# Optimization experiments

Hardware: AMD Instinct MI355X
Metric: run time of the kernel (lower is better)

## Reference

```python
import jax, jax.numpy as jnp
import numpy as np

DIM = 512
HEADS = 8
HEAD_DIM = DIM // HEADS
SCALE = HEAD_DIM ** -0.5
B, H, W = 8, 64, 64


def rotate_every_two(x):
    # interleaved pair rotation: (x0,x1,x2,x3,...) -> (-x1,x0,-x3,x2,...)
    x1 = x[..., ::2]
    x2 = x[..., 1::2]
    return jnp.stack([-x2, x1], axis=-1).reshape(x.shape)


def theta_shift(x, sin, cos):
    return x * cos + rotate_every_two(x) * sin


def setup_inputs() -> dict:
    key = jax.random.key(0)
    ks = jax.random.split(key, 6)
    N = H * W
    x = jax.random.normal(ks[0], (B, DIM, H, W), jnp.float32)
    sin = jax.random.uniform(ks[1], (N, HEAD_DIM), jnp.float32, minval=-1.0, maxval=1.0)
    cos = jax.random.uniform(ks[2], (N, HEAD_DIM), jnp.float32, minval=-1.0, maxval=1.0)
    w_qkvo = jax.random.normal(ks[3], (4 * DIM, DIM), jnp.float32) * (DIM ** -0.5)
    b_qkvo = jnp.zeros((4 * DIM,), jnp.float32)
    w_lepe = jax.random.normal(ks[4], (DIM, 1, 5, 5), jnp.float32) * 0.1
    b_lepe = jnp.zeros((DIM,), jnp.float32)
    w_proj = jax.random.normal(ks[5], (DIM, DIM), jnp.float32) * (DIM ** -0.5)
    b_proj = jnp.zeros((DIM,), jnp.float32)
    return dict(x=x, sin=sin, cos=cos, w_qkvo=w_qkvo, b_qkvo=b_qkvo,
                w_lepe=w_lepe, b_lepe=b_lepe, w_proj=w_proj, b_proj=b_proj)


def reference(x, sin, cos, w_qkvo, b_qkvo, w_lepe, b_lepe, w_proj, b_proj):
    Bx, C, Hx, Wx = x.shape
    N = Hx * Wx
    # 1x1 conv qkvo projection
    qkvo = jnp.einsum('bchw,oc->bohw', x, w_qkvo) + b_qkvo[None, :, None, None]
    qkv = qkvo[:, :3 * DIM]
    o = qkvo[:, 3 * DIM:]
    # depthwise 5x5 lepe on v (spatial layout)
    v_sp = qkv[:, 2 * DIM:3 * DIM]
    lepe = jax.lax.conv_general_dilated(
        v_sp, w_lepe, window_strides=(1, 1), padding=((2, 2), (2, 2)),
        dimension_numbers=('NCHW', 'OIHW', 'NCHW'), feature_group_count=DIM,
    ) + b_lepe[None, :, None, None]
    # b (3 n d) h w -> (3, b, n, N, d)
    qkv5 = qkv.reshape(Bx, 3, HEADS, HEAD_DIM, N).transpose(1, 0, 2, 4, 3)
    q, k, v = qkv5[0], qkv5[1], qkv5[2]
    q = jax.nn.elu(q) + 1.0
    k = jax.nn.elu(k) + 1.0
    # softmax-gated eff weighting of k
    q_mean = q.mean(axis=-2, keepdims=True)                       # (b,n,1,d)
    eff = SCALE * jnp.einsum('bnod,bntd->bnot', q_mean, k)        # (b,n,1,N)
    eff = jax.nn.softmax(eff, axis=-1).swapaxes(-1, -2)           # (b,n,N,1)
    k = k * eff * N
    # RoPE-style rotation
    q_rope = theta_shift(q, sin, cos)
    k_rope = theta_shift(k, sin, cos)
    # normalizer z (uses un-rotated q, gated k)
    z = 1.0 / (jnp.einsum('bntd,bnod->bnto', q, k.mean(axis=-2, keepdims=True)) + 1e-6)  # (b,n,N,1)
    # linear-attention kv accumulation (d x d)
    inv_sqrt_n = N ** -0.5
    kv = jnp.einsum('bntd,bnte->bnde', k_rope * inv_sqrt_n, v * inv_sqrt_n)  # (b,n,d,d)
    res = jnp.einsum('bntd,bnde->bnte', q_rope, kv) * z            # (b,n,N,d)
    # b n N d -> b (n d) h w
    res = res.transpose(0, 1, 3, 2).reshape(Bx, DIM, Hx, Wx)
    res = res + lepe
    out = jnp.einsum('bchw,oc->bohw', res * o, w_proj) + b_proj[None, :, None, None]
    return out
```

## Files before the change

### kernel.cpp

```cpp
#include <hip/hip_runtime.h>
#include <math.h>

#define N_SP 4096
#define DIMC 512
#define HEADS 8
#define HD 64
#define CH_STRIDE 1536

typedef __attribute__((ext_vector_type(8))) short short8;
typedef __attribute__((ext_vector_type(4))) float f32x4;

__device__ __forceinline__ float elu1(float x) { return x > 0.f ? x + 1.f : expf(x); }

__device__ __forceinline__ float waveSum(float v) {
#pragma unroll
    for (int o = 1; o < 64; o <<= 1) v += __shfl_xor(v, o);
    return v;
}
__device__ __forceinline__ float waveMax(float v) {
#pragma unroll
    for (int o = 1; o < 64; o <<= 1) v = fmaxf(v, __shfl_xor(v, o));
    return v;
}

__device__ __forceinline__ unsigned short f2bf(float f) {
    union { float f; unsigned u; } v; v.f = f;
    unsigned r = v.u + 0x7fffu + ((v.u >> 16) & 1u);
    return (unsigned short)(r >> 16);
}
__device__ __forceinline__ unsigned pk2(float lo, float hi) {
    return (unsigned)f2bf(lo) | ((unsigned)f2bf(hi) << 16);
}

template<bool GATED>
__global__ __launch_bounds__(256) void gemm_bf16(
    const float* __restrict__ W, const float* __restrict__ bias,
    const float* __restrict__ Bsrc, const float* __restrict__ Gsrc,
    float* __restrict__ C, int src_cstride, int dst_cstride)
{
    __shared__ unsigned short Ws[4096];
    __shared__ unsigned short Xs[4096];
    int b  = blockIdx.z;
    int bo = blockIdx.y * 128;
    int bn = blockIdx.x * 128;
    const float* Bb = Bsrc + (size_t)b * src_cstride * N_SP + bn;
    const float* Gb = GATED ? (Gsrc + (size_t)b * src_cstride * N_SP + bn) : nullptr;
    int tid  = threadIdx.x;
    int lane = tid & 63;
    int wid  = tid >> 6;
    int wm = (wid >> 1) * 64, wn = (wid & 1) * 64;
    int quad = lane >> 4, l16 = lane & 15;
    int sm = tid >> 1, sp = tid & 1;
    int xn = tid & 127, xk0 = tid >> 7;

    f32x4 acc[4][4];
#pragma unroll
    for (int i = 0; i < 4; i++)
#pragma unroll
        for (int j = 0; j < 4; j++) acc[i][j] = f32x4{0.f, 0.f, 0.f, 0.f};

    for (int c0 = 0; c0 < DIMC; c0 += 32) {
        const float* wp = W + (size_t)(bo + sm) * DIMC + c0 + sp * 16;
        float4 w0 = *(const float4*)(wp);
        float4 w1 = *(const float4*)(wp + 4);
        float4 w2 = *(const float4*)(wp + 8);
        float4 w3 = *(const float4*)(wp + 12);
        float xv[2][8];
#pragma unroll
        for (int g = 0; g < 2; g++) {
            int kb = xk0 + g * 2;
            const float* xp = Bb + (size_t)(c0 + kb * 8) * N_SP + xn;
#pragma unroll
            for (int i = 0; i < 8; i++) xv[g][i] = xp[(size_t)i * N_SP];
            if (GATED) {
                const float* gp = Gb + (size_t)(c0 + kb * 8) * N_SP + xn;
#pragma unroll
                for (int i = 0; i < 8; i++) xv[g][i] *= gp[(size_t)i * N_SP];
            }
        }
        if (c0) __syncthreads();
        {
            uint4 a, bq;
            a.x  = pk2(w0.x, w0.y); a.y  = pk2(w0.z, w0.w);
            a.z  = pk2(w1.x, w1.y); a.w  = pk2(w1.z, w1.w);
            bq.x = pk2(w2.x, w2.y); bq.y = pk2(w2.z, w2.w);
            bq.z = pk2(w3.x, w3.y); bq.w = pk2(w3.z, w3.w);
            *(uint4*)&Ws[(2 * sp)     * 1024 + sm * 8] = a;
            *(uint4*)&Ws[(2 * sp + 1) * 1024 + sm * 8] = bq;
        }
#pragma unroll
        for (int g = 0; g < 2; g++) {
            int kb = xk0 + g * 2;
            uint4 a;
            a.x = pk2(xv[g][0], xv[g][1]); a.y = pk2(xv[g][2], xv[g][3]);
            a.z = pk2(xv[g][4], xv[g][5]); a.w = pk2(xv[g][6], xv[g][7]);
            *(uint4*)&Xs[kb * 1024 + xn * 8] = a;
        }
        __syncthreads();
        short8 af[4], bf[4];
#pragma unroll
        for (int i = 0; i < 4; i++) {
            af[i] = *(const short8*)&Ws[quad * 1024 + (wm + i * 16 + l16) * 8];
            bf[i] = *(const short8*)&Xs[quad * 1024 + (wn + i * 16 + l16) * 8];
        }
#pragma unroll
        for (int i = 0; i < 4; i++)
#pragma unroll
            for (int j = 0; j < 4; j++)
                acc[i][j] = __builtin_amdgcn_mfma_f32_16x16x32_bf16(
                    af[i], bf[j], acc[i][j], 0, 0, 0);
    }
    float* Cb = C + (size_t)b * dst_cstride * N_SP;
#pragma unroll
    for (int i = 0; i < 4; i++) {
        int row0 = bo + wm + i * 16 + quad * 4;
#pragma unroll
        for (int r = 0; r < 4; r++) {
            float bi = bias[row0 + r];
            float* cr = Cb + (size_t)(row0 + r) * N_SP + bn + wn + l16;
#pragma unroll
            for (int j = 0; j < 4; j++)
                cr[j * 16] = acc[i][j][r] + bi;
        }
    }
}

__global__ __launch_bounds__(256) void qmean_kernel(
    const float* __restrict__ QKV, float* __restrict__ qmean)
{
    int d = blockIdx.x, h = blockIdx.y, b = blockIdx.z;
    const float* row = QKV + ((size_t)b * CH_STRIDE + h * 64 + d) * N_SP;
    int tid = threadIdx.x;
    float s = 0.f;
#pragma unroll
    for (int j = 0; j < 4; j++) {
        float4 v = ((const float4*)row)[j * 256 + tid];
        s += elu1(v.x) + elu1(v.y) + elu1(v.z) + elu1(v.w);
    }
    s = waveSum(s);
    __shared__ float red[4];
    if ((tid & 63) == 0) red[tid >> 6] = s;
    __syncthreads();
    if (tid == 0)
        qmean[((size_t)b * 8 + h) * 64 + d] = (red[0] + red[1] + red[2] + red[3]) * (1.f / N_SP);
}

__global__ __launch_bounds__(256) void logits_kernel(
    const float* __restrict__ QKV, const float* __restrict__ qmean,
    float* __restrict__ eff)
{
    int tc = blockIdx.x, h = blockIdx.y, b = blockIdx.z;
    int tid = threadIdx.x;
    int t = tc * 256 + tid;
    __shared__ float qm[64];
    if (tid < 64) qm[tid] = qmean[((size_t)b * 8 + h) * 64 + tid];
    __syncthreads();
    const float* kb = QKV + ((size_t)b * CH_STRIDE + 512 + h * 64) * N_SP;
    float s = 0.f;
#pragma unroll 8
    for (int d = 0; d < 64; d++) s += qm[d] * elu1(kb[(size_t)d * N_SP + t]);
    eff[((size_t)b * 8 + h) * N_SP + t] = 0.125f * s;
}

__global__ __launch_bounds__(256) void softmax_kernel(float* __restrict__ eff)
{
    int bh = blockIdx.x;
    float* row = eff + (size_t)bh * N_SP;
    int tid = threadIdx.x;
    float4 v[4];
#pragma unroll
    for (int j = 0; j < 4; j++) v[j] = ((float4*)row)[j * 256 + tid];
    float m = -1e30f;
#pragma unroll
    for (int j = 0; j < 4; j++)
        m = fmaxf(m, fmaxf(fmaxf(v[j].x, v[j].y), fmaxf(v[j].z, v[j].w)));
    m = waveMax(m);
    __shared__ float red[8];
    if ((tid & 63) == 0) red[tid >> 6] = m;
    __syncthreads();
    m = fmaxf(fmaxf(red[0], red[1]), fmaxf(red[2], red[3]));
    float s = 0.f;
#pragma unroll
    for (int j = 0; j < 4; j++) {
        v[j].x = expf(v[j].x - m); v[j].y = expf(v[j].y - m);
        v[j].z = expf(v[j].z - m); v[j].w = expf(v[j].w - m);
        s += v[j].x + v[j].y + v[j].z + v[j].w;
    }
    float ws = waveSum(s);
    if ((tid & 63) == 0) red[4 + (tid >> 6)] = ws;
    __syncthreads();
    float tot = red[4] + red[5] + red[6] + red[7];
    float sc = (float)N_SP / tot;
#pragma unroll
    for (int j = 0; j < 4; j++) {
        v[j].x *= sc; v[j].y *= sc; v[j].z *= sc; v[j].w *= sc;
        ((float4*)row)[j * 256 + tid] = v[j];
    }
}

__global__ __launch_bounds__(256) void kv_kernel(
    const float* __restrict__ QKV, const float* __restrict__ eff,
    const float* __restrict__ sinp, const float* __restrict__ cosp,
    float* __restrict__ kv, float* __restrict__ kmean)
{
    int sp = blockIdx.x;
    int h = blockIdx.y, b = blockIdx.z;
    int bh = b * 8 + h;
    int tid = threadIdx.x;
    int r = tid >> 2, quad = tid & 3;
    const float* krow = QKV + ((size_t)b * CH_STRIDE + 512 + h * 64 + r) * N_SP;
    const float* vrow = QKV + ((size_t)b * CH_STRIDE + 1024 + h * 64 + r) * N_SP;
    const float* prow = eff + (size_t)bh * N_SP;
    __shared__ float ksr[64 * 65];
    __shared__ float vs[64 * 65];
    int dg = tid >> 4, eg = tid & 15;
    float acc[4][4];
#pragma unroll
    for (int i = 0; i < 4; i++)
#pragma unroll
        for (int j = 0; j < 4; j++) acc[i][j] = 0.f;
    float km = 0.f;
    float sgn = (r & 1) ? 1.f : -1.f;

    for (int c = 0; c < 8; c++) {
        int t0 = sp * 512 + c * 64;
        int tb = t0 + quad * 16;
        float kx[16], vv[16];
#pragma unroll
        for (int i4 = 0; i4 < 4; i4++) {
            float4 kf = *(const float4*)(krow + tb + i4 * 4);
            float4 pf = *(const float4*)(prow + tb + i4 * 4);
            float4 vf = *(const float4*)(vrow + tb + i4 * 4);
            kx[i4 * 4 + 0] = elu1(kf.x) * pf.x;
            kx[i4 * 4 + 1] = elu1(kf.y) * pf.y;
            kx[i4 * 4 + 2] = elu1(kf.z) * pf.z;
            kx[i4 * 4 + 3] = elu1(kf.w) * pf.w;
            vv[i4 * 4 + 0] = vf.x; vv[i4 * 4 + 1] = vf.y;
            vv[i4 * 4 + 2] = vf.z; vv[i4 * 4 + 3] = vf.w;
        }
#pragma unroll
        for (int i = 0; i < 16; i++) km += kx[i];
        __syncthreads();
#pragma unroll
        for (int i = 0; i < 16; i++) {
            float partner = __shfl_xor(kx[i], 4);
            int t = tb + i;
            float sv = sinp[(size_t)t * 64 + r];
            float cv = cosp[(size_t)t * 64 + r];
            float kr = kx[i] * cv + sgn * partner * sv;
            ksr[r * 65 + (t - t0)] = kr;
            vs[r * 65 + (t - t0)] = vv[i];
        }
        __syncthreads();
#pragma unroll 8
        for (int t = 0; t < 64; t++) {
            float a[4], bb[4];
#pragma unroll
            for (int i = 0; i < 4; i++) a[i] = ksr[(dg * 4 + i) * 65 + t];
#pragma unroll
            for (int j = 0; j < 4; j++) bb[j] = vs[(eg * 4 + j) * 65 + t];
#pragma unroll
            for (int i = 0; i < 4; i++)
#pragma unroll
                for (int j = 0; j < 4; j++) acc[i][j] += a[i] * bb[j];
        }
    }
#pragma unroll
    for (int i = 0; i < 4; i++)
#pragma unroll
        for (int j = 0; j < 4; j++)
            atomicAdd(&kv[((size_t)bh * 64 + dg * 4 + i) * 64 + eg * 4 + j],
                      acc[i][j] * (1.f / N_SP));
    km += __shfl_xor(km, 1);
    km += __shfl_xor(km, 2);
    if (quad == 0) atomicAdd(&kmean[(size_t)bh * 64 + r], km * (1.f / N_SP));
}

__global__ __launch_bounds__(256) void res_kernel(
    const float* __restrict__ QKV, const float* __restrict__ kv,
    const float* __restrict__ kmean,
    const float* __restrict__ sinp, const float* __restrict__ cosp,
    float* __restrict__ res)
{
    int tc = blockIdx.x;
    int h = blockIdx.y, b = blockIdx.z;
    int bh = b * 8 + h;
    int tid = threadIdx.x;
    int t0 = tc * 64;
    __shared__ float qsr[64 * 65];
    __shared__ float qse[64 * 65];
    __shared__ float kvs[64 * 65];
    __shared__ float zs[64];
    __shared__ float kms[64];
#pragma unroll
    for (int j = 0; j < 16; j++) {
        int lin = j * 256 + tid;
        kvs[(lin >> 6) * 65 + (lin & 63)] = kv[(size_t)bh * 4096 + lin];
    }
    if (tid < 64) kms[tid] = kmean[(size_t)bh * 64 + tid];

    int r = tid >> 2, quad = tid & 3;
    const float* qrow = QKV + ((size_t)b * CH_STRIDE + h * 64 + r) * N_SP;
    float sgn = (r & 1) ? 1.f : -1.f;
    int tb = t0 + quad * 16;
#pragma unroll
    for (int i4 = 0; i4 < 4; i4++) {
        float4 qf = *(const float4*)(qrow + tb + i4 * 4);
        float qe[4] = { elu1(qf.x), elu1(qf.y), elu1(qf.z), elu1(qf.w) };
#pragma unroll
        for (int ii = 0; ii < 4; ii++) {
            float partner = __shfl_xor(qe[ii], 4);
            int t = tb + i4 * 4 + ii;
            float sv = sinp[(size_t)t * 64 + r];
            float cv = cosp[(size_t)t * 64 + r];
            qse[r * 65 + (t - t0)] = qe[ii];
            qsr[r * 65 + (t - t0)] = qe[ii] * cv + sgn * partner * sv;
        }
    }
    __syncthreads();
    if (tid < 64) {
        float s = 0.f;
#pragma unroll 8
        for (int d = 0; d < 64; d++) s += qse[d * 65 + tid] * kms[d];
        zs[tid] = 1.f / (s + 1e-6f);
    }
    __syncthreads();

    int eg = tid >> 4, tg = tid & 15;
    float acc[4][4];
#pragma unroll
    for (int j = 0; j < 4; j++)
#pragma unroll
        for (int i = 0; i < 4; i++) acc[j][i] = 0.f;
#pragma unroll 4
    for (int d = 0; d < 64; d++) {
        float qv[4], kvv[4];
#pragma unroll
        for (int i = 0; i < 4; i++) qv[i] = qsr[d * 65 + tg * 4 + i];
#pragma unroll
        for (int j = 0; j < 4; j++) kvv[j] = kvs[d * 65 + eg * 4 + j];
#pragma unroll
        for (int j = 0; j < 4; j++)
#pragma unroll
            for (int i = 0; i < 4; i++) acc[j][i] += kvv[j] * qv[i];
    }
    float* rb = res + ((size_t)b * CH_STRIDE + 512 + h * 64) * N_SP;
#pragma unroll
    for (int j = 0; j < 4; j++) {
        float4 o4;
        o4.x = acc[j][0] * zs[tg * 4 + 0];
        o4.y = acc[j][1] * zs[tg * 4 + 1];
        o4.z = acc[j][2] * zs[tg * 4 + 2];
        o4.w = acc[j][3] * zs[tg * 4 + 3];
        *(float4*)(rb + (size_t)(eg * 4 + j) * N_SP + t0 + tg * 4) = o4;
    }
}

#define LPS 73
__global__ __launch_bounds__(256) void lepe_kernel(
    const float* __restrict__ QKV, const float* __restrict__ wl,
    const float* __restrict__ bl, float* __restrict__ res)
{
    int c = blockIdx.x & 511;
    int b = blockIdx.x >> 9;
    __shared__ float img[68 * LPS];
    int tid = threadIdx.x;
    const float* vb = QKV + ((size_t)b * CH_STRIDE + 1024 + c) * N_SP;

    for (int i = tid; i < 68 * LPS; i += 256) img[i] = 0.f;
    __syncthreads();
#pragma unroll
    for (int i = 0; i < 4; i++) {
        int p = i * 256 + tid;
        float4 v4 = ((const float4*)vb)[p];
        int y = p >> 4;
        int x = (p & 15) * 4;
        float* dst = &img[(y + 2) * LPS + (x + 2)];
        dst[0] = v4.x; dst[1] = v4.y; dst[2] = v4.z; dst[3] = v4.w;
    }
    float w[25];
    const float* wc = wl + c * 25;
#pragma unroll
    for (int i = 0; i < 25; i++) w[i] = wc[i];
    float bias = bl[c];
    __syncthreads();

    int y  = tid >> 2;
    int x0 = (tid & 3) * 16;
    float acc[16];
#pragma unroll
    for (int u = 0; u < 16; u++) acc[u] = bias;
#pragma unroll
    for (int i = 0; i < 5; i++) {
        float rowv[20];
#pragma unroll
        for (int q = 0; q < 20; q++)
            rowv[q] = img[(y + i) * LPS + x0 + q];
#pragma unroll
        for (int j = 0; j < 5; j++)
#pragma unroll
            for (int u = 0; u < 16; u++)
                acc[u] += rowv[u + j] * w[i * 5 + j];
    }
    float* rr = res + ((size_t)b * CH_STRIDE + 512 + c) * N_SP + y * 64 + x0;
#pragma unroll
    for (int q = 0; q < 4; q++) {
        float4 r4 = *(const float4*)&rr[q * 4];
        r4.x += acc[q * 4 + 0]; r4.y += acc[q * 4 + 1];
        r4.z += acc[q * 4 + 2]; r4.w += acc[q * 4 + 3];
        *(float4*)&rr[q * 4] = r4;
    }
}

extern "C" void kernel_launch(void* const* d_in, const int* in_sizes, int n_in,
                              void* d_out, int out_size, void* d_ws, size_t ws_size,
                              hipStream_t stream)
{
    const float* x      = (const float*)d_in[0];
    const float* sinp   = (const float*)d_in[1];
    const float* cosp   = (const float*)d_in[2];
    const float* w_qkvo = (const float*)d_in[3];
    const float* b_qkvo = (const float*)d_in[4];
    const float* w_lepe = (const float*)d_in[5];
    const float* b_lepe = (const float*)d_in[6];
    const float* w_proj = (const float*)d_in[7];
    const float* b_proj = (const float*)d_in[8];
    float* out = (float*)d_out;
    float* ws  = (float*)d_ws;

    float* qkv   = ws;
    float* eff   = ws + 50331648;
    float* qmean = ws + 50593792;
    float* kmean = ws + 50597888;
    float* kv    = ws + 50601984;

    hipMemsetAsync(kmean, 0, (4096 + 262144) * sizeof(float), stream);

    gemm_bf16<false><<<dim3(32, 12, 8), 256, 0, stream>>>(
        w_qkvo, b_qkvo, x, nullptr, qkv, DIMC, CH_STRIDE);
    qmean_kernel<<<dim3(64, 8, 8), 256, 0, stream>>>(qkv, qmean);
    logits_kernel<<<dim3(16, 8, 8), 256, 0, stream>>>(qkv, qmean, eff);
    softmax_kernel<<<64, 256, 0, stream>>>(eff);
    kv_kernel<<<dim3(8, 8, 8), 256, 0, stream>>>(qkv, eff, sinp, cosp, kv, kmean);
    res_kernel<<<dim3(64, 8, 8), 256, 0, stream>>>(qkv, kv, kmean, sinp, cosp, qkv);
    lepe_kernel<<<4096, 256, 0, stream>>>(qkv, w_lepe, b_lepe, qkv);
    gemm_bf16<false><<<dim3(32, 4, 8), 256, 0, stream>>>(
        w_qkvo + 1536 * DIMC, b_qkvo + 1536, x, nullptr, qkv, DIMC, CH_STRIDE);
    gemm_bf16<true><<<dim3(32, 4, 8), 256, 0, stream>>>(
        w_proj, b_proj, qkv + (size_t)512 * N_SP, qkv, out, CH_STRIDE, DIMC);
}
```

Measured before the change: 570.8 us.

## Pre-convert x and weights to bf16 and load GEMM tiles via global_load_lds

```diff
diff --git a/kernel.cpp b/kernel.cpp
--- a/kernel.cpp
+++ b/kernel.cpp
@@ -9,6 +9,7 @@
 
 typedef __attribute__((ext_vector_type(8))) short short8;
 typedef __attribute__((ext_vector_type(4))) float f32x4;
+typedef unsigned short ushortx;
 
 __device__ __forceinline__ float elu1(float x) { return x > 0.f ? x + 1.f : expf(x); }
 
@@ -32,8 +33,104 @@
     return (unsigned)f2bf(lo) | ((unsigned)f2bf(hi) << 16);
 }
 
-template<bool GATED>
-__global__ __launch_bounds__(256) void gemm_bf16(
+__device__ __forceinline__ void gl_lds16(const unsigned short* g, unsigned short* l) {
+    __builtin_amdgcn_global_load_lds(
+        (const __attribute__((address_space(1))) unsigned int*)g,
+        (__attribute__((address_space(3))) unsigned int*)l, 16, 0, 0);
+}
+
+__global__ __launch_bounds__(256) void cvt_xT(
+    const float* __restrict__ x, unsigned short* __restrict__ xT)
+{
+    int n  = blockIdx.x * 256 + threadIdx.x;
+    int c0 = blockIdx.y * 128;
+    int b  = blockIdx.z;
+    const float* xb = x + ((size_t)b * DIMC + c0) * N_SP + n;
+    unsigned short* xo = xT + ((size_t)b * N_SP + n) * DIMC + c0;
+    for (int cc = 0; cc < 128; cc += 8) {
+        float v[8];
+#pragma unroll
+        for (int i = 0; i < 8; i++) v[i] = xb[(size_t)(cc + i) * N_SP];
+        uint4 p;
+        p.x = pk2(v[0], v[1]); p.y = pk2(v[2], v[3]);
+        p.z = pk2(v[4], v[5]); p.w = pk2(v[6], v[7]);
+        *(uint4*)&xo[cc] = p;
+    }
+}
+
+__global__ __launch_bounds__(256) void cvt_wb(
+    const float* __restrict__ w, unsigned short* __restrict__ wb, int n4)
+{
+    int i = blockIdx.x * 256 + threadIdx.x;
+    if (i < n4) {
+        float4 v = ((const float4*)w)[i];
+        uint2 p; p.x = pk2(v.x, v.y); p.y = pk2(v.z, v.w);
+        *(uint2*)&wb[(size_t)i * 4] = p;
+    }
+}
+
+__global__ __launch_bounds__(256) void gemm_bb(
+    const unsigned short* __restrict__ Wb, const float* __restrict__ bias,
+    const unsigned short* __restrict__ xT, float* __restrict__ C,
+    int dst_cstride)
+{
+    __shared__ __align__(16) unsigned short Ws[4096];
+    __shared__ __align__(16) unsigned short Xs[4096];
+    int b  = blockIdx.z;
+    int bo = blockIdx.y * 128;
+    int bn = blockIdx.x * 128;
+    const unsigned short* Xb = xT + ((size_t)b * N_SP + bn) * DIMC;
+    int tid  = threadIdx.x;
+    int lane = tid & 63;
+    int wid  = tid >> 6;
+    int wm = (wid >> 1) * 64, wn = (wid & 1) * 64;
+    int quad = lane >> 4, l16 = lane & 15;
+
+    f32x4 acc[4][4];
+#pragma unroll
+    for (int i = 0; i < 4; i++)
+#pragma unroll
+        for (int j = 0; j < 4; j++) acc[i][j] = f32x4{0.f, 0.f, 0.f, 0.f};
+
+    for (int c0 = 0; c0 < DIMC; c0 += 32) {
+        if (c0) __syncthreads();
+#pragma unroll
+        for (int r = 0; r < 2; r++) {
+            gl_lds16(Wb + (size_t)(bo + r * 64 + lane) * DIMC + c0 + wid * 8,
+                     &Ws[wid * 1024 + r * 512]);
+            gl_lds16(Xb + (size_t)(r * 64 + lane) * DIMC + c0 + wid * 8,
+                     &Xs[wid * 1024 + r * 512]);
+        }
+        __syncthreads();
+        short8 af[4], bf[4];
+#pragma unroll
+        for (int i = 0; i < 4; i++) {
+            af[i] = *(const short8*)&Ws[quad * 1024 + (wm + i * 16 + l16) * 8];
+            bf[i] = *(const short8*)&Xs[quad * 1024 + (wn + i * 16 + l16) * 8];
+        }
+#pragma unroll
+        for (int i = 0; i < 4; i++)
+#pragma unroll
+            for (int j = 0; j < 4; j++)
+                acc[i][j] = __builtin_amdgcn_mfma_f32_16x16x32_bf16(
+                    af[i], bf[j], acc[i][j], 0, 0, 0);
+    }
+    float* Cb = C + (size_t)b * dst_cstride * N_SP;
+#pragma unroll
+    for (int i = 0; i < 4; i++) {
+        int row0 = bo + wm + i * 16 + quad * 4;
+#pragma unroll
+        for (int r = 0; r < 4; r++) {
+            float bi = bias[row0 + r];
+            float* cr = Cb + (size_t)(row0 + r) * N_SP + bn + wn + l16;
+#pragma unroll
+            for (int j = 0; j < 4; j++)
+                cr[j * 16] = acc[i][j][r] + bi;
+        }
+    }
+}
+
+__global__ __launch_bounds__(256) void gemm_gated_f32(
     const float* __restrict__ W, const float* __restrict__ bias,
     const float* __restrict__ Bsrc, const float* __restrict__ Gsrc,
     float* __restrict__ C, int src_cstride, int dst_cstride)
@@ -44,7 +141,7 @@
     int bo = blockIdx.y * 128;
     int bn = blockIdx.x * 128;
     const float* Bb = Bsrc + (size_t)b * src_cstride * N_SP + bn;
-    const float* Gb = GATED ? (Gsrc + (size_t)b * src_cstride * N_SP + bn) : nullptr;
+    const float* Gb = Gsrc + (size_t)b * src_cstride * N_SP + bn;
     int tid  = threadIdx.x;
     int lane = tid & 63;
     int wid  = tid >> 6;
@@ -70,13 +167,10 @@
         for (int g = 0; g < 2; g++) {
             int kb = xk0 + g * 2;
             const float* xp = Bb + (size_t)(c0 + kb * 8) * N_SP + xn;
-#pragma unroll
-            for (int i = 0; i < 8; i++) xv[g][i] = xp[(size_t)i * N_SP];
-            if (GATED) {
-                const float* gp = Gb + (size_t)(c0 + kb * 8) * N_SP + xn;
-#pragma unroll
-                for (int i = 0; i < 8; i++) xv[g][i] *= gp[(size_t)i * N_SP];
-            }
+            const float* gp = Gb + (size_t)(c0 + kb * 8) * N_SP + xn;
+#pragma unroll
+            for (int i = 0; i < 8; i++)
+                xv[g][i] = xp[(size_t)i * N_SP] * gp[(size_t)i * N_SP];
         }
         if (c0) __syncthreads();
         {
@@ -434,18 +528,23 @@
     float* kmean = ws + 50597888;
     float* kv    = ws + 50601984;
 
+    unsigned short* xT = (unsigned short*)d_out;
+    unsigned short* wb = (unsigned short*)d_out + 16777216;
+
     hipMemsetAsync(kmean, 0, (4096 + 262144) * sizeof(float), stream);
 
-    gemm_bf16<false><<<dim3(32, 12, 8), 256, 0, stream>>>(
-        w_qkvo, b_qkvo, x, nullptr, qkv, DIMC, CH_STRIDE);
+    cvt_wb<<<1024, 256, 0, stream>>>(w_qkvo, wb, 2048 * DIMC / 4);
+    cvt_xT<<<dim3(16, 4, 8), 256, 0, stream>>>(x, xT);
+
+    gemm_bb<<<dim3(32, 12, 8), 256, 0, stream>>>(wb, b_qkvo, xT, qkv, CH_STRIDE);
     qmean_kernel<<<dim3(64, 8, 8), 256, 0, stream>>>(qkv, qmean);
     logits_kernel<<<dim3(16, 8, 8), 256, 0, stream>>>(qkv, qmean, eff);
     softmax_kernel<<<64, 256, 0, stream>>>(eff);
     kv_kernel<<<dim3(8, 8, 8), 256, 0, stream>>>(qkv, eff, sinp, cosp, kv, kmean);
     res_kernel<<<dim3(64, 8, 8), 256, 0, stream>>>(qkv, kv, kmean, sinp, cosp, qkv);
     lepe_kernel<<<4096, 256, 0, stream>>>(qkv, w_lepe, b_lepe, qkv);
-    gemm_bf16<false><<<dim3(32, 4, 8), 256, 0, stream>>>(
-        w_qkvo + 1536 * DIMC, b_qkvo + 1536, x, nullptr, qkv, DIMC, CH_STRIDE);
-    gemm_bf16<true><<<dim3(32, 4, 8), 256, 0, stream>>>(
+    gemm_bb<<<dim3(32, 4, 8), 256, 0, stream>>>(
+        wb + (size_t)1536 * DIMC, b_qkvo + 1536, xT, qkv, CH_STRIDE);
+    gemm_gated_f32<<<dim3(32, 4, 8), 256, 0, stream>>>(
         w_proj, b_proj, qkv + (size_t)512 * N_SP, qkv, out, CH_STRIDE, DIMC);
 }
```

After: 588.2 us. 3.1% more time.
